# Optimization experiments

Hardware: AMD Instinct MI355X
Metric: run time of the kernel (lower is better)

The kernel has to match this reference:

```python
import jax, jax.numpy as jnp
import numpy as np

CHEB_K = 3
ORDER = 2


def setup_inputs() -> dict:
    key = jax.random.key(0)
    ks = jax.random.split(key, 7)
    B, C, N, T = 16, 64, 2048, 12
    E, O = 10, 64
    x = jax.random.normal(ks[0], (B, C, N, T), jnp.float32)
    node_embeddings = jax.random.normal(ks[1], (N, E), jnp.float32)
    # nonnegative row-normalized adjacency for the diffusion branch
    a = jax.random.uniform(ks[2], (1, N, N), jnp.float32)
    support = a / jnp.sum(a, axis=-1, keepdims=True)
    weights_pool = 0.05 * jax.random.normal(ks[3], (E, CHEB_K, C, O), jnp.float32)
    bias_pool = 0.05 * jax.random.normal(ks[4], (E, O), jnp.float32)
    mlp_w = 0.05 * jax.random.normal(ks[5], ((ORDER * 1 + 1) * C, O), jnp.float32)
    mlp_b = 0.05 * jax.random.normal(ks[6], (O,), jnp.float32)
    return {
        "x": x,
        "node_embeddings": node_embeddings,
        "support": support,
        "weights_pool": weights_pool,
        "bias_pool": bias_pool,
        "mlp_w": mlp_w,
        "mlp_b": mlp_b,
    }


def reference(x, node_embeddings, support, weights_pool, bias_pool, mlp_w, mlp_b):
    # ---- adaptive Chebyshev branch ----
    N = node_embeddings.shape[0]
    A = jax.nn.softmax(jax.nn.relu(node_embeddings @ node_embeddings.T), axis=1)  # [N,N]
    supports = [jnp.eye(N, dtype=A.dtype), A]
    for _ in range(2, CHEB_K):
        supports.append(2.0 * (A @ supports[-1]) - supports[-2])
    S = jnp.stack(supports, axis=0)                         # [K,N,N]
    weights = jnp.einsum('nd,dkio->nkio', node_embeddings, weights_pool)  # [N,K,C,O]
    bias = node_embeddings @ bias_pool                      # [N,O]
    # x: [B,C,N,T]; diffuse then contract per-node weights
    x_g = jnp.einsum('knm,bimw->bwnki', S, x)               # [B,T,N,K,C]
    x_av = jnp.einsum('bwnki,nkio->bwno', x_g, weights) + bias  # [B,T,N,O]
    x_av = x_av.transpose(0, 3, 2, 1)                       # [B,O,N,T]

    # ---- diffusion conv branch ----
    out = [x]
    for si in range(support.shape[0]):
        a = support[si]                                     # [N,N]
        x1 = jnp.einsum('bcvl,vw->bcwl', x, a)
        out.append(x1)
        for _ in range(2, ORDER + 1):
            x1 = jnp.einsum('bcvl,vw->bcwl', x1, a)
            out.append(x1)
    xg = jnp.concatenate(out, axis=1)                       # [B,(order*S+1)*C,N,T]
    # 1x1 Conv2d == channel matmul; dropout is identity in eval mode
    x_gcn = jnp.einsum('bcnw,co->bonw', xg, mlp_w) + mlp_b[None, :, None, None]
    return x_av, x_gcn
```

## Files before the change

kernel.cpp:

```cpp
#include <hip/hip_runtime.h>
#include <stdint.h>

#define NN    2048
#define BB    16
#define CC    64
#define TT    12
#define OO    64
#define ED    10
#define JJ    12288
#define NJ    25165824
#define MBT   192
#define KC    192

typedef __attribute__((ext_vector_type(8))) short short8;
typedef __attribute__((ext_vector_type(4))) float f32x4;

__device__ __forceinline__ unsigned short f2bf(float x) {
    union { float f; unsigned int u; } v; v.f = x;
    unsigned int r = (v.u + 0x7FFFu + ((v.u >> 16) & 1u)) >> 16;
    return (unsigned short)r;
}
__device__ __forceinline__ float bf2f(unsigned short h) {
    union { unsigned int u; float f; } v; v.u = ((unsigned int)h) << 16;
    return v.f;
}
__device__ __forceinline__ void async_cp16(const void* g, void* l) {
    __builtin_amdgcn_global_load_lds(
        (const __attribute__((address_space(1))) void*)(uintptr_t)g,
        (__attribute__((address_space(3))) void*)(uintptr_t)l, 16, 0, 0);
}

__global__ __launch_bounds__(256) void k_softmax_A(const float* __restrict__ E,
                                                   unsigned short* __restrict__ Abf) {
    int n = blockIdx.x, tid = threadIdx.x;
    __shared__ float row[NN];
    __shared__ float red[256];
    float en[ED];
#pragma unroll
    for (int d = 0; d < ED; ++d) en[d] = E[n * ED + d];
    float mx = 0.0f;
    for (int m = tid; m < NN; m += 256) {
        float s = 0.f;
#pragma unroll
        for (int d = 0; d < ED; ++d) s += en[d] * E[m * ED + d];
        s = fmaxf(s, 0.0f);
        row[m] = s;
        mx = fmaxf(mx, s);
    }
    red[tid] = mx; __syncthreads();
    for (int s = 128; s; s >>= 1) { if (tid < s) red[tid] = fmaxf(red[tid], red[tid + s]); __syncthreads(); }
    mx = red[0]; __syncthreads();
    float sum = 0.f;
    for (int m = tid; m < NN; m += 256) { float e = __expf(row[m] - mx); row[m] = e; sum += e; }
    red[tid] = sum; __syncthreads();
    for (int s = 128; s; s >>= 1) { if (tid < s) red[tid] += red[tid + s]; __syncthreads(); }
    float inv = 1.0f / red[0];
    for (int m = tid; m < NN; m += 256) Abf[(size_t)n * NN + m] = f2bf(row[m] * inv);
}

__global__ void k_trans_bf(const float* __restrict__ src, unsigned short* __restrict__ dst) {
    __shared__ float t[32][33];
    int tx = threadIdx.x, ty = threadIdx.y;
    int x0 = blockIdx.x * 32, y0 = blockIdx.y * 32;
#pragma unroll
    for (int i = 0; i < 4; ++i)
        t[ty + i * 8][tx] = src[(size_t)(y0 + ty + i * 8) * NN + x0 + tx];
    __syncthreads();
#pragma unroll
    for (int i = 0; i < 4; ++i)
        dst[(size_t)(x0 + ty + i * 8) * NN + y0 + tx] = f2bf(t[tx][ty + i * 8]);
}

__global__ __launch_bounds__(256) void k_make_X2(const float* __restrict__ x,
                                                 unsigned short* __restrict__ X2) {
    int idx = blockIdx.x * 256 + threadIdx.x;
    int n = idx / JJ;
    int r = idx - n * JJ;
    int bt = r >> 6;
    int c = r & 63;
    int b = bt / TT;
    int t = bt - b * TT;
    X2[idx] = f2bf(x[(((size_t)b * CC + c) * NN + n) * TT + t]);
}

__global__ __launch_bounds__(256) void k_gemm(const unsigned short* __restrict__ Am,
                                              const unsigned short* __restrict__ Bm,
                                              unsigned short* __restrict__ Out,
                                              const unsigned short* __restrict__ Csub,
                                              float alpha) {
    __shared__ __align__(16) unsigned short lA[128 * 32];
    __shared__ __align__(16) unsigned short lB[128 * 40];
    int tid = threadIdx.x, lane = tid & 63, wv = tid >> 6;
    int m0 = blockIdx.y * 128, j0 = blockIdx.x * 128;
    int wm = (wv >> 1) * 64, wn = (wv & 1) * 64;
    f32x4 zero = {0.f, 0.f, 0.f, 0.f};
    f32x4 acc[4][4];
#pragma unroll
    for (int a = 0; a < 4; ++a)
#pragma unroll
        for (int b = 0; b < 4; ++b) acc[a][b] = zero;

    int bj = (tid >> 4) * 8;
    int bk = (tid & 15) * 2;
    int q = lane >> 4, l15 = lane & 15;

    for (int kt = 0; kt < 64; ++kt) {
        int k0 = kt * 32;
        __syncthreads();
#pragma unroll
        for (int c = 0; c < 2; ++c) {
            int rowA = (wv + 4 * c) * 16 + (lane >> 2);
            int kkA = (lane & 3) * 8;
            async_cp16(Am + (size_t)(m0 + rowA) * 2048 + k0 + kkA,
                       &lA[(size_t)(wv + 4 * c) * 512 + lane * 8]);
        }
        {
            const unsigned short* g0 = Bm + (size_t)(k0 + bk) * JJ + j0 + bj;
            uint4 r0 = *(const uint4*)g0;
            uint4 r1 = *(const uint4*)(g0 + JJ);
            unsigned int* lB32 = (unsigned int*)lB;
            const unsigned int* p0 = &r0.x;
            const unsigned int* p1 = &r1.x;
#pragma unroll
            for (int i = 0; i < 8; ++i) {
                unsigned int lo = (i & 1) ? (p0[i >> 1] >> 16) : (p0[i >> 1] & 0xFFFFu);
                unsigned int hi = (i & 1) ? (p1[i >> 1] >> 16) : (p1[i >> 1] & 0xFFFFu);
                lB32[((bj + i) * 40 + bk) >> 1] = lo | (hi << 16);
            }
        }
        __syncthreads();
        short8 af[4], bfr[4];
#pragma unroll
        for (int tm = 0; tm < 4; ++tm)
            af[tm] = *(const short8*)&lA[(wm + tm * 16 + l15) * 32 + q * 8];
#pragma unroll
        for (int tn = 0; tn < 4; ++tn)
            bfr[tn] = *(const short8*)&lB[(wn + tn * 16 + l15) * 40 + q * 8];
#pragma unroll
        for (int tm = 0; tm < 4; ++tm)
#pragma unroll
            for (int tn = 0; tn < 4; ++tn)
                acc[tm][tn] = __builtin_amdgcn_mfma_f32_16x16x32_bf16(af[tm], bfr[tn], acc[tm][tn], 0, 0, 0);
    }
#pragma unroll
    for (int tm = 0; tm < 4; ++tm) {
#pragma unroll
        for (int tn = 0; tn < 4; ++tn) {
            int mm = m0 + wm + tm * 16 + q * 4;
            int jj = j0 + wn + tn * 16 + l15;
#pragma unroll
            for (int r = 0; r < 4; ++r) {
                size_t oidx = (size_t)(mm + r) * JJ + jj;
                float v = alpha * acc[tm][tn][r];
                if (Csub) v -= bf2f(Csub[oidx]);
                Out[oidx] = f2bf(v);
            }
        }
    }
}

__global__ __launch_bounds__(256) void k_node(const unsigned short* __restrict__ S0,
                                              const unsigned short* __restrict__ S1,
                                              const unsigned short* __restrict__ S2,
                                              const float* __restrict__ E,
                                              const float* __restrict__ Wp,
                                              const float* __restrict__ bias_pool,
                                              const float* __restrict__ mlp_w,
                                              const float* __restrict__ mlp_b,
                                              float* __restrict__ out,
                                              int branch) {
    int n = blockIdx.x, tid = threadIdx.x, lane = tid & 63, wv = tid >> 6;
    __shared__ __align__(16) unsigned short lW[64 * 200];
    __shared__ __align__(16) unsigned short lS[192 * 72];
    __shared__ float lBias[64];
    int q = lane >> 4, l15 = lane & 15;

    if (branch == 0) {
        float en[ED];
#pragma unroll
        for (int d = 0; d < ED; ++d) en[d] = E[n * ED + d];
        for (int idx = tid; idx < KC * OO; idx += 256) {
            int o = idx & 63, kap = idx >> 6;
            float s = 0.f;
#pragma unroll
            for (int d = 0; d < ED; ++d) s += en[d] * Wp[((size_t)d * KC + kap) * OO + o];
            lW[o * 200 + kap] = f2bf(s);
        }
        if (tid < 64) {
            float s = 0.f;
#pragma unroll
            for (int d = 0; d < ED; ++d) s += en[d] * bias_pool[d * OO + tid];
            lBias[tid] = s;
        }
    } else {
        for (int idx = tid; idx < KC * OO; idx += 256) {
            int o = idx & 63, kap = idx >> 6;
            lW[o * 200 + kap] = f2bf(mlp_w[kap * OO + o]);
        }
        if (tid < 64) lBias[tid] = mlp_b[tid];
    }

    f32x4 zero = {0.f, 0.f, 0.f, 0.f};
    f32x4 acc[3][4];
#pragma unroll
    for (int a = 0; a < 3; ++a)
#pragma unroll
        for (int b = 0; b < 4; ++b) acc[a][b] = zero;

    const unsigned short* Ss[3] = { S0 + (size_t)n * JJ, S1 + (size_t)n * JJ, S2 + (size_t)n * JJ };

    for (int s = 0; s < 3; ++s) {
        __syncthreads();
#pragma unroll
        for (int v = 0; v < 6; ++v) {
            int e8 = (v * 256 + tid) * 8;
            int m = e8 >> 6, i = e8 & 63;
            *(short8*)&lS[m * 72 + i] = *(const short8*)&Ss[s][e8];
        }
        __syncthreads();
#pragma unroll
        for (int h = 0; h < 2; ++h) {
            short8 af[3], bfr[4];
#pragma unroll
            for (int tm = 0; tm < 3; ++tm)
                af[tm] = *(const short8*)&lS[(wv * 48 + tm * 16 + l15) * 72 + h * 32 + q * 8];
#pragma unroll
            for (int tn = 0; tn < 4; ++tn)
                bfr[tn] = *(const short8*)&lW[(tn * 16 + l15) * 200 + s * 64 + h * 32 + q * 8];
#pragma unroll
            for (int tm = 0; tm < 3; ++tm)
#pragma unroll
                for (int tn = 0; tn < 4; ++tn)
                    acc[tm][tn] = __builtin_amdgcn_mfma_f32_16x16x32_bf16(af[tm], bfr[tn], acc[tm][tn], 0, 0, 0);
        }
    }
#pragma unroll
    for (int tm = 0; tm < 3; ++tm) {
#pragma unroll
        for (int tn = 0; tn < 4; ++tn) {
            int o = tn * 16 + l15;
#pragma unroll
            for (int r = 0; r < 4; ++r) {
                int m = wv * 48 + tm * 16 + q * 4 + r;
                int b = m / TT, t = m - b * TT;
                out[(((size_t)b * OO + o) * NN + n) * TT + t] = acc[tm][tn][r] + lBias[o];
            }
        }
    }
}

extern "C" void kernel_launch(void* const* d_in, const int* in_sizes, int n_in,
                              void* d_out, int out_size, void* d_ws, size_t ws_size,
                              hipStream_t stream) {
    const float* x         = (const float*)d_in[0];
    const float* node_emb  = (const float*)d_in[1];
    const float* support   = (const float*)d_in[2];
    const float* wpool     = (const float*)d_in[3];
    const float* bpool     = (const float*)d_in[4];
    const float* mlp_w     = (const float*)d_in[5];
    const float* mlp_b     = (const float*)d_in[6];
    float* out             = (float*)d_out;

    unsigned short* Abf = (unsigned short*)d_ws;
    unsigned short* Atb = Abf + (size_t)NN * NN;
    unsigned short* X2  = Atb + (size_t)NN * NN;
    unsigned short* Y1  = X2 + (size_t)NJ;
    unsigned short* Y2  = Y1 + (size_t)NJ;
    unsigned short* Z1  = Y2 + (size_t)NJ;
    unsigned short* Z2  = Z1 + (size_t)NJ;

    k_softmax_A<<<NN, 256, 0, stream>>>(node_emb, Abf);
    k_trans_bf<<<dim3(64, 64), dim3(32, 8), 0, stream>>>(support, Atb);
    k_make_X2<<<NJ / 256, 256, 0, stream>>>(x, X2);

    dim3 gg(96, 16);
    k_gemm<<<gg, 256, 0, stream>>>(Abf, X2, Y1, nullptr, 1.0f);
    k_gemm<<<gg, 256, 0, stream>>>(Abf, Y1, Y2, X2, 2.0f);
    k_gemm<<<gg, 256, 0, stream>>>(Atb, X2, Z1, nullptr, 1.0f);
    k_gemm<<<gg, 256, 0, stream>>>(Atb, Z1, Z2, nullptr, 1.0f);

    k_node<<<NN, 256, 0, stream>>>(X2, Y1, Y2, node_emb, wpool, bpool, nullptr, nullptr,
                                   out, 0);
    k_node<<<NN, 256, 0, stream>>>(X2, Z1, Z2, nullptr, nullptr, nullptr, mlp_w, mlp_b,
                                   out + (size_t)NJ, 1);
}
```

Baseline: 1.152 ms.

## Pre-transpose GEMM B operands so both tiles load via async LDS copies

Adds a bf16 transpose kernel and feeds each GEMM a K-contiguous copy of its right-hand operand. Both A and B tiles can then be staged with global_load_lds 16-byte copies, replacing the register load plus 16-bit repacking and padded LDS layout for B. The schedule is reordered to reuse five workspace buffers, and each branch's node kernel runs right after its GEMMs. The cost is three extra transpose passes over 48 MB tensors, and the unpadded LDS B layout may cause bank conflicts.

```diff
diff --git a/kernel.cpp b/kernel.cpp
--- a/kernel.cpp
+++ b/kernel.cpp
@@ -9,7 +9,6 @@
 #define ED    10
 #define JJ    12288
 #define NJ    25165824
-#define MBT   192
 #define KC    192
 
 typedef __attribute__((ext_vector_type(8))) short short8;
@@ -83,13 +82,35 @@
     X2[idx] = f2bf(x[(((size_t)b * CC + c) * NN + n) * TT + t]);
 }
 
+__global__ __launch_bounds__(256) void k_trans16(const unsigned short* __restrict__ src,
+                                                 unsigned short* __restrict__ dst) {
+    __shared__ unsigned short t[64][72];
+    int tid = threadIdx.x;
+    int j0 = blockIdx.x * 64, n0 = blockIdx.y * 64;
+    int r = tid >> 3, c8 = (tid & 7) * 8;
+#pragma unroll
+    for (int it = 0; it < 2; ++it) {
+        int rr = r + it * 32;
+        *(short8*)&t[rr][c8] = *(const short8*)&src[(size_t)(n0 + rr) * JJ + j0 + c8];
+    }
+    __syncthreads();
+#pragma unroll
+    for (int it = 0; it < 2; ++it) {
+        int rr = r + it * 32;
+        unsigned short v[8];
+#pragma unroll
+        for (int u = 0; u < 8; ++u) v[u] = t[c8 + u][rr];
+        *(short8*)&dst[(size_t)(j0 + rr) * NN + n0 + c8] = *(short8*)v;
+    }
+}
+
 __global__ __launch_bounds__(256) void k_gemm(const unsigned short* __restrict__ Am,
-                                              const unsigned short* __restrict__ Bm,
+                                              const unsigned short* __restrict__ Bt,
                                               unsigned short* __restrict__ Out,
                                               const unsigned short* __restrict__ Csub,
                                               float alpha) {
     __shared__ __align__(16) unsigned short lA[128 * 32];
-    __shared__ __align__(16) unsigned short lB[128 * 40];
+    __shared__ __align__(16) unsigned short lB[128 * 32];
     int tid = threadIdx.x, lane = tid & 63, wv = tid >> 6;
     int m0 = blockIdx.y * 128, j0 = blockIdx.x * 128;
     int wm = (wv >> 1) * 64, wn = (wv & 1) * 64;
@@ -100,33 +121,21 @@
 #pragma unroll
         for (int b = 0; b < 4; ++b) acc[a][b] = zero;
 
-    int bj = (tid >> 4) * 8;
-    int bk = (tid & 15) * 2;
     int q = lane >> 4, l15 = lane & 15;
+    int rA = lane >> 2;
+    int cA = (lane & 3) * 8;
+
+    const unsigned short* gA = Am + (size_t)(m0 + (lane >> 2)) * 2048 + cA;
+    const unsigned short* gB = Bt + (size_t)(j0 + (lane >> 2)) * 2048 + cA;
 
     for (int kt = 0; kt < 64; ++kt) {
         int k0 = kt * 32;
         __syncthreads();
 #pragma unroll
         for (int c = 0; c < 2; ++c) {
-            int rowA = (wv + 4 * c) * 16 + (lane >> 2);
-            int kkA = (lane & 3) * 8;
-            async_cp16(Am + (size_t)(m0 + rowA) * 2048 + k0 + kkA,
-                       &lA[(size_t)(wv + 4 * c) * 512 + lane * 8]);
-        }
-        {
-            const unsigned short* g0 = Bm + (size_t)(k0 + bk) * JJ + j0 + bj;
-            uint4 r0 = *(const uint4*)g0;
-            uint4 r1 = *(const uint4*)(g0 + JJ);
-            unsigned int* lB32 = (unsigned int*)lB;
-            const unsigned int* p0 = &r0.x;
-            const unsigned int* p1 = &r1.x;
-#pragma unroll
-            for (int i = 0; i < 8; ++i) {
-                unsigned int lo = (i & 1) ? (p0[i >> 1] >> 16) : (p0[i >> 1] & 0xFFFFu);
-                unsigned int hi = (i & 1) ? (p1[i >> 1] >> 16) : (p1[i >> 1] & 0xFFFFu);
-                lB32[((bj + i) * 40 + bk) >> 1] = lo | (hi << 16);
-            }
+            int g = wv + 4 * c;
+            async_cp16(gA + (size_t)g * 16 * 2048 + k0, &lA[g * 512 + lane * 8]);
+            async_cp16(gB + (size_t)g * 16 * 2048 + k0, &lB[g * 512 + lane * 8]);
         }
         __syncthreads();
         short8 af[4], bfr[4];
@@ -135,7 +144,7 @@
             af[tm] = *(const short8*)&lA[(wm + tm * 16 + l15) * 32 + q * 8];
 #pragma unroll
         for (int tn = 0; tn < 4; ++tn)
-            bfr[tn] = *(const short8*)&lB[(wn + tn * 16 + l15) * 40 + q * 8];
+            bfr[tn] = *(const short8*)&lB[(wn + tn * 16 + l15) * 32 + q * 8];
 #pragma unroll
         for (int tm = 0; tm < 4; ++tm)
 #pragma unroll
@@ -263,24 +272,29 @@
 
     unsigned short* Abf = (unsigned short*)d_ws;
     unsigned short* Atb = Abf + (size_t)NN * NN;
-    unsigned short* X2  = Atb + (size_t)NN * NN;
-    unsigned short* Y1  = X2 + (size_t)NJ;
-    unsigned short* Y2  = Y1 + (size_t)NJ;
-    unsigned short* Z1  = Y2 + (size_t)NJ;
-    unsigned short* Z2  = Z1 + (size_t)NJ;
+    unsigned short* b1  = Atb + (size_t)NN * NN;
+    unsigned short* b2  = b1 + (size_t)NJ;
+    unsigned short* b3  = b2 + (size_t)NJ;
+    unsigned short* b4  = b3 + (size_t)NJ;
+    unsigned short* b5  = b4 + (size_t)NJ;
+
+    dim3 gg(96, 16);
+    dim3 gt(192, 32);
 
     k_softmax_A<<<NN, 256, 0, stream>>>(node_emb, Abf);
     k_trans_bf<<<dim3(64, 64), dim3(32, 8), 0, stream>>>(support, Atb);
-    k_make_X2<<<NJ / 256, 256, 0, stream>>>(x, X2);
-
-    dim3 gg(96, 16);
-    k_gemm<<<gg, 256, 0, stream>>>(Abf, X2, Y1, nullptr, 1.0f);
-    k_gemm<<<gg, 256, 0, stream>>>(Abf, Y1, Y2, X2, 2.0f);
-    k_gemm<<<gg, 256, 0, stream>>>(Atb, X2, Z1, nullptr, 1.0f);
-    k_gemm<<<gg, 256, 0, stream>>>(Atb, Z1, Z2, nullptr, 1.0f);
-
-    k_node<<<NN, 256, 0, stream>>>(X2, Y1, Y2, node_emb, wpool, bpool, nullptr, nullptr,
+    k_make_X2<<<NJ / 256, 256, 0, stream>>>(x, b2);
+    k_trans16<<<gt, 256, 0, stream>>>(b2, b1);
+
+    k_gemm<<<gg, 256, 0, stream>>>(Abf, b1, b4, nullptr, 1.0f);
+    k_trans16<<<gt, 256, 0, stream>>>(b4, b3);
+    k_gemm<<<gg, 256, 0, stream>>>(Abf, b3, b5, b2, 2.0f);
+    k_node<<<NN, 256, 0, stream>>>(b2, b4, b5, node_emb, wpool, bpool, nullptr, nullptr,
                                    out, 0);
-    k_node<<<NN, 256, 0, stream>>>(X2, Z1, Z2, nullptr, nullptr, nullptr, mlp_w, mlp_b,
+
+    k_gemm<<<gg, 256, 0, stream>>>(Atb, b1, b4, nullptr, 1.0f);
+    k_trans16<<<gt, 256, 0, stream>>>(b4, b3);
+    k_gemm<<<gg, 256, 0, stream>>>(Atb, b3, b5, nullptr, 1.0f);
+    k_node<<<NN, 256, 0, stream>>>(b2, b4, b5, nullptr, nullptr, nullptr, mlp_w, mlp_b,
                                    out + (size_t)NJ, 1);
 }
```

Measured after the change: 1.112 ms. -3.5%, faster.
